# Performance work log

Hardware: AMD Instinct MI355X
Metric: run time of the kernel (lower is better)

The kernel has to match this reference:

```python
import jax, jax.numpy as jnp
import numpy as np

B, T, C, H, HS = 128, 256, 384, 6, 64

def setup_inputs() -> dict:
    key = jax.random.key(0)
    k1, k2, k3, k4, k5 = jax.random.split(key, 5)
    s = 0.02
    return {
        "x": jax.random.normal(k1, (B, T, C), dtype=jnp.float32),
        "Wq": jax.random.normal(k2, (H, C, HS), dtype=jnp.float32) * s,
        "Wk": jax.random.normal(k3, (H, C, HS), dtype=jnp.float32) * s,
        "Wv": jax.random.normal(k4, (H, C, HS), dtype=jnp.float32) * s,
        "Wp": jax.random.normal(k5, (C, C), dtype=jnp.float32) * s,
        "bp": jnp.zeros((C,), dtype=jnp.float32),
    }

def reference(x, Wq, Wk, Wv, Wp, bp):
    # per-head projections: [B,H,T,HS]
    q = jnp.einsum('btc,hcd->bhtd', x, Wq)
    k = jnp.einsum('btc,hcd->bhtd', x, Wk)
    v = jnp.einsum('btc,hcd->bhtd', x, Wv)
    scale = 1.0 / jnp.sqrt(jnp.asarray(HS, dtype=x.dtype))
    # scores: [B,H,T,T], causal mask then stable softmax
    scores = jnp.einsum('bhtd,bhsd->bhts', q, k) * scale
    causal = jnp.tril(jnp.ones((T, T), dtype=bool))
    scores = jnp.where(causal, scores, -jnp.inf)
    wei = jax.nn.softmax(scores, axis=-1)
    # dropout is identity in eval mode
    out = jnp.einsum('bhts,bhsd->bhtd', wei, v)  # [B,H,T,HS]
    out = out.transpose(0, 2, 1, 3).reshape(B, T, H * HS)  # concat heads
    return out @ Wp.T + bp  # output projection
```

## Files before the change

### kernel.cpp

```cpp
#include <hip/hip_runtime.h>
#include <hip/hip_bf16.h>
#include <math.h>

#define B_   128
#define T_   256
#define C_   384
#define H_   6
#define HS_  64
#define NTOK (B_*T_)
#define NQKV (3*C_)

typedef unsigned short u16;
typedef __attribute__((ext_vector_type(8))) short bf16x8;
typedef __attribute__((ext_vector_type(4))) float f32x4;

__device__ __forceinline__ u16 f2b(float f) {
    unsigned int u = __builtin_bit_cast(unsigned int, f);
    unsigned int r = (u + 0x7FFFu + ((u >> 16) & 1u)) >> 16;
    return (u16)r;
}

__device__ __forceinline__ float fexp2(float x) {
#if __has_builtin(__builtin_amdgcn_exp2f)
    return __builtin_amdgcn_exp2f(x);
#else
    return exp2f(x);
#endif
}

__device__ __forceinline__ void gl2lds16(const u16* g, u16* l) {
    __builtin_amdgcn_global_load_lds(
        (const __attribute__((address_space(1))) unsigned int*)g,
        (__attribute__((address_space(3))) unsigned int*)l, 16, 0, 0);
}

#define QSCALE 0.180336880f

#define J0_ (NTOK*C_/8)
#define J2_ (C_*C_/8)
#define J1_ (NQKV*C_)

__global__ __launch_bounds__(256) void prep(
    const float* __restrict__ x,  const float* __restrict__ Wq,
    const float* __restrict__ Wk, const float* __restrict__ Wv,
    const float* __restrict__ Wp,
    u16* __restrict__ xb, u16* __restrict__ wct, u16* __restrict__ wpb)
{
    int i = blockIdx.x * 256 + threadIdx.x;
    if (i < J0_) {
        const float4* s = (const float4*)x + (size_t)i * 2;
        float4 a = s[0], b = s[1];
        ushort4 o1, o2;
        o1.x = f2b(a.x); o1.y = f2b(a.y); o1.z = f2b(a.z); o1.w = f2b(a.w);
        o2.x = f2b(b.x); o2.y = f2b(b.y); o2.z = f2b(b.z); o2.w = f2b(b.w);
        ((ushort4*)xb)[(size_t)i * 2]     = o1;
        ((ushort4*)xb)[(size_t)i * 2 + 1] = o2;
    } else if (i < J0_ + J2_) {
        int j = i - J0_;
        const float4* s = (const float4*)Wp + (size_t)j * 2;
        float4 a = s[0], b = s[1];
        ushort4 o1, o2;
        o1.x = f2b(a.x); o1.y = f2b(a.y); o1.z = f2b(a.z); o1.w = f2b(a.w);
        o2.x = f2b(b.x); o2.y = f2b(b.y); o2.z = f2b(b.z); o2.w = f2b(b.w);
        ((ushort4*)wpb)[(size_t)j * 2]     = o1;
        ((ushort4*)wpb)[(size_t)j * 2 + 1] = o2;
    } else {
        int j = i - J0_ - J2_;
        if (j < J1_) {
            int n = j / C_, c = j % C_;
            int h = n / 192, rem = n % 192;
            int p = rem >> 6, d = rem & 63;
            const float* W = (p == 0 ? Wq : (p == 1 ? Wk : Wv));
            wct[j] = f2b(W[(h * C_ + c) * HS_ + d]);
        }
    }
}

__global__ __launch_bounds__(512, 2) void qkv_attn(
    const u16* __restrict__ xb, const u16* __restrict__ wct,
    u16* __restrict__ yb)
{
    __shared__ __align__(16) u16 SM[40960];
    u16* R0 = SM;
    u16* R1 = SM + 16384;
    u16* R2 = SM + 32768;

    const int gid = blockIdx.x;
    const int lin = (gid & 7) * 96 + (gid >> 3);
    const int b = lin / 6, h = lin % 6;

    const int tid = threadIdx.x;
    const int w = tid >> 6, lane = tid & 63;
    const int lm = lane & 15, qd = lane >> 4;
    const int wm = (w >> 1) * 64, wn = (w & 1) * 96;

    const int schunk = (lane & 7) ^ ((lane >> 3) & 7);
    const u16* gA = xb  + (size_t)(b * T_ + w * 32 + (lane >> 3)) * C_ + schunk * 8;
    const u16* gB = wct + (size_t)(h * 192 + w * 24 + (lane >> 3)) * C_ + schunk * 8;
    u16* lA = &R0[(w * 32) * 64];
    u16* lB = &R1[(w * 24) * 64];

    f32x4 acc[4][6];
    #pragma unroll
    for (int mi = 0; mi < 4; ++mi)
        #pragma unroll
        for (int ni = 0; ni < 6; ++ni)
            acc[mi][ni] = (f32x4){0.f, 0.f, 0.f, 0.f};

    for (int k0 = 0; k0 < C_; k0 += 64) {
        __syncthreads();
        #pragma unroll
        for (int j = 0; j < 4; ++j)
            gl2lds16(gA + j * 8 * C_, lA + j * 8 * 64);
        #pragma unroll
        for (int j = 0; j < 3; ++j)
            gl2lds16(gB + j * 8 * C_, lB + j * 8 * 64);
        gA += 64; gB += 64;
        __syncthreads();

        #pragma unroll
        for (int ks = 0; ks < 2; ++ks) {
            bf16x8 af[4], bfr[6];
            #pragma unroll
            for (int mi = 0; mi < 4; ++mi) {
                const int row = wm + mi * 16 + lm;
                const int sl = (ks * 4 + qd) ^ (lm & 7);
                af[mi] = *(const bf16x8*)&R0[row * 64 + sl * 8];
            }
            #pragma unroll
            for (int ni = 0; ni < 6; ++ni) {
                const int row = wn + ni * 16 + lm;
                const int sl = (ks * 4 + qd) ^ (lm & 7);
                bfr[ni] = *(const bf16x8*)&R1[row * 64 + sl * 8];
            }
            #pragma unroll
            for (int mi = 0; mi < 4; ++mi)
                #pragma unroll
                for (int ni = 0; ni < 6; ++ni)
                    acc[mi][ni] = __builtin_amdgcn_mfma_f32_16x16x32_bf16(
                        af[mi], bfr[ni], acc[mi][ni], 0, 0, 0);
        }
    }

    __syncthreads();
    #pragma unroll
    for (int mi = 0; mi < 4; ++mi) {
        const int t0 = wm + mi * 16 + qd * 4;
        #pragma unroll
        for (int ni = 0; ni < 6; ++ni) {
            const int n = wn + ni * 16 + lm;
            if (n < 64) {
                #pragma unroll
                for (int r = 0; r < 4; ++r) {
                    const int t = t0 + r;
                    R1[t * 64 + (((n >> 3) ^ (t & 7)) << 3) + (n & 7)]
                        = f2b(acc[mi][ni][r] * QSCALE);
                }
            } else if (n >= 128) {
                const int d = n - 128;
                const int ch = t0 >> 3;
                const int pos = (ch & 16) | ((ch ^ (d & 15)) & 15);
                ushort4 sv;
                sv.x = f2b(acc[mi][ni][0]); sv.y = f2b(acc[mi][ni][1]);
                sv.z = f2b(acc[mi][ni][2]); sv.w = f2b(acc[mi][ni][3]);
                *(ushort4*)&R0[d * 256 + pos * 8 + (t0 & 7)] = sv;
            }
        }
    }
    __syncthreads();

    const int trg0 = w * 16;
    const int trg1 = 128 + (7 - w) * 16;
    bf16x8 aq[2][2];
    #pragma unroll
    for (int rg = 0; rg < 2; ++rg) {
        const int t = (rg ? trg1 : trg0) + lm;
        #pragma unroll
        for (int ks = 0; ks < 2; ++ks)
            aq[rg][ks] = *(const bf16x8*)
                &R1[t * 64 + (((ks * 4 + qd) ^ (t & 7)) << 3)];
    }
    __syncthreads();

    #pragma unroll
    for (int mi = 0; mi < 4; ++mi) {
        const int t0 = wm + mi * 16 + qd * 4;
        #pragma unroll
        for (int ni = 0; ni < 6; ++ni) {
            const int n = wn + ni * 16 + lm;
            if (n >= 64 && n < 128) {
                const int d = n - 64;
                #pragma unroll
                for (int r = 0; r < 4; ++r) {
                    const int t = t0 + r;
                    R1[t * 64 + (((d >> 3) ^ (t & 7)) << 3) + (d & 7)]
                        = f2b(acc[mi][ni][r]);
                }
            }
        }
    }
    __syncthreads();

    f32x4 oacc[2][4];
    float ms[2][4], ls[2][4];
    #pragma unroll
    for (int rg = 0; rg < 2; ++rg) {
        #pragma unroll
        for (int ni = 0; ni < 4; ++ni) oacc[rg][ni] = (f32x4){0.f, 0.f, 0.f, 0.f};
        #pragma unroll
        for (int r = 0; r < 4; ++r) { ms[rg][r] = -INFINITY; ls[rg][r] = 0.f; }
    }

    u16* Pw = R2 + w * 1024;

    #pragma unroll
    for (int rg = 0; rg < 2; ++rg) {
        const int trg = rg ? trg1 : trg0;
        const int kmax = (trg + 15) >> 6;
        for (int kt = 0; kt <= kmax; ++kt) {
            const int j0 = kt * 64;
            const bool needmask = (j0 + 63 > trg);

            f32x4 st[4];
            #pragma unroll
            for (int ni = 0; ni < 4; ++ni) st[ni] = (f32x4){0.f, 0.f, 0.f, 0.f};
            #pragma unroll
            for (int ks = 0; ks < 2; ++ks) {
                #pragma unroll
                for (int ni = 0; ni < 4; ++ni) {
                    const int krow = j0 + ni * 16 + lm;
                    const int sl = (ks * 4 + qd) ^ (lm & 7);
                    bf16x8 bk = *(const bf16x8*)&R1[krow * 64 + sl * 8];
                    st[ni] = __builtin_amdgcn_mfma_f32_16x16x32_bf16(
                        aq[rg][ks], bk, st[ni], 0, 0, 0);
                }
            }

            float vals[4][4], rowmax[4];
            #pragma unroll
            for (int r = 0; r < 4; ++r) rowmax[r] = -INFINITY;
            #pragma unroll
            for (int ni = 0; ni < 4; ++ni) {
                const int s_g = j0 + ni * 16 + lm;
                #pragma unroll
                for (int r = 0; r < 4; ++r) {
                    float sc = st[ni][r];
                    if (needmask) {
                        const int t_g = trg + qd * 4 + r;
                        sc = (s_g > t_g) ? -1e30f : sc;
                    }
                    vals[ni][r] = sc;
                    rowmax[r] = fmaxf(rowmax[r], sc);
                }
            }
            #pragma unroll
            for (int msk = 1; msk <= 8; msk <<= 1)
                #pragma unroll
                for (int r = 0; r < 4; ++r)
                    rowmax[r] = fmaxf(rowmax[r], __shfl_xor(rowmax[r], msk, 64));

            float corr[4], rowsum[4];
            #pragma unroll
            for (int r = 0; r < 4; ++r) {
                const float mn = fmaxf(ms[rg][r], rowmax[r]);
                corr[r] = fexp2(ms[rg][r] - mn);
                ms[rg][r] = mn;
                rowsum[r] = 0.f;
            }
            #pragma unroll
            for (int ni = 0; ni < 4; ++ni) {
                #pragma unroll
                for (int r = 0; r < 4; ++r) {
                    const float pv = fexp2(vals[ni][r] - ms[rg][r]);
                    rowsum[r] += pv;
                    const int prow = qd * 4 + r;
                    const int pcol = ni * 16 + lm;
                    const int pch  = (pcol >> 3) ^ (prow & 7);
                    Pw[prow * 64 + pch * 8 + (pcol & 7)] = f2b(pv);
                }
            }
            #pragma unroll
            for (int msk = 1; msk <= 8; msk <<= 1)
                #pragma unroll
                for (int r = 0; r < 4; ++r)
                    rowsum[r] += __shfl_xor(rowsum[r], msk, 64);
            #pragma unroll
            for (int r = 0; r < 4; ++r) ls[rg][r] = ls[rg][r] * corr[r] + rowsum[r];
            #pragma unroll
            for (int ni = 0; ni < 4; ++ni)
                #pragma unroll
                for (int r = 0; r < 4; ++r)
                    oacc[rg][ni][r] *= corr[r];

            #pragma unroll
            for (int ks = 0; ks < 2; ++ks) {
                const int rch = (ks * 4 + qd) ^ (lm & 7);
                bf16x8 pa = *(const bf16x8*)&Pw[lm * 64 + rch * 8];
                #pragma unroll
                for (int ni = 0; ni < 4; ++ni) {
                    const int d = ni * 16 + lm;
                    const int cj = kt * 8 + ks * 4 + qd;
                    const int pos = (cj & 16) | ((cj ^ (d & 15)) & 15);
                    bf16x8 bv = *(const bf16x8*)&R0[d * 256 + pos * 8];
                    oacc[rg][ni] = __builtin_amdgcn_mfma_f32_16x16x32_bf16(
                        pa, bv, oacc[rg][ni], 0, 0, 0);
                }
            }
        }
    }

    __syncthreads();
    u16 (*yt)[72] = (u16(*)[72])SM;
    #pragma unroll
    for (int rg = 0; rg < 2; ++rg) {
        const int trow = (rg ? trg1 : trg0) + qd * 4;
        #pragma unroll
        for (int r = 0; r < 4; ++r) {
            const float inv = 1.f / ls[rg][r];
            #pragma unroll
            for (int ni = 0; ni < 4; ++ni)
                yt[trow + r][ni * 16 + lm] = f2b(oacc[rg][ni][r] * inv);
        }
    }
    __syncthreads();
    #pragma unroll
    for (int rr = 0; rr < 4; ++rr) {
        const int row = rr * 64 + (tid >> 3);
        const int col = (tid & 7) * 8;
        bf16x8 vv = *(const bf16x8*)&yt[row][col];
        *(bf16x8*)(yb + ((size_t)(b * T_ + row)) * C_ + h * 64 + col) = vv;
    }
}

__global__ __launch_bounds__(512, 4) void gemm_proj(
    const u16* __restrict__ yb, const u16* __restrict__ wpb,
    const float* __restrict__ bp, float* __restrict__ out)
{
    __shared__ __align__(16) u16 SMEM[256 * 64 + 128 * 64];
    u16* As = SMEM;
    u16* Bs = SMEM + 256 * 64;

    const int gid  = blockIdx.x;
    const int xcd  = gid & 7;
    const int j_   = gid >> 3;
    const int colb = j_ % 3;
    const int rowb = (j_ / 3) * 8 + xcd;
    const int m0g  = rowb * 256;
    const int n0g  = colb * 128;

    const int tid = threadIdx.x;
    const int w = tid >> 6, lane = tid & 63;
    const int lm = lane & 15, qd = lane >> 4;
    const int wm = (w >> 1) * 64, wn = (w & 1) * 64;

    const int schunk = (lane & 7) ^ ((lane >> 3) & 7);
    const u16* gA = yb  + (size_t)(m0g + w * 32 + (lane >> 3)) * C_ + schunk * 8;
    const u16* gB = wpb + (size_t)(n0g + w * 16 + (lane >> 3)) * C_ + schunk * 8;
    u16* lA = &As[(w * 32) * 64];
    u16* lB = &Bs[(w * 16) * 64];

    f32x4 acc[4][4];
    #pragma unroll
    for (int mi = 0; mi < 4; ++mi)
        #pragma unroll
        for (int ni = 0; ni < 4; ++ni)
            acc[mi][ni] = (f32x4){0.f, 0.f, 0.f, 0.f};

    for (int k0 = 0; k0 < C_; k0 += 64) {
        __syncthreads();
        #pragma unroll
        for (int j = 0; j < 4; ++j)
            gl2lds16(gA + j * 8 * C_, lA + j * 8 * 64);
        #pragma unroll
        for (int j = 0; j < 2; ++j)
            gl2lds16(gB + j * 8 * C_, lB + j * 8 * 64);
        gA += 64; gB += 64;
        __syncthreads();

        #pragma unroll
        for (int ks = 0; ks < 2; ++ks) {
            bf16x8 af[4], bfr[4];
            #pragma unroll
            for (int mi = 0; mi < 4; ++mi) {
                const int row = wm + mi * 16 + lm;
                const int sl = (ks * 4 + qd) ^ (lm & 7);
                af[mi] = *(const bf16x8*)&As[row * 64 + sl * 8];
            }
            #pragma unroll
            for (int ni = 0; ni < 4; ++ni) {
                const int row = wn + ni * 16 + lm;
                const int sl = (ks * 4 + qd) ^ (lm & 7);
                bfr[ni] = *(const bf16x8*)&Bs[row * 64 + sl * 8];
            }
            #pragma unroll
            for (int mi = 0; mi < 4; ++mi)
                #pragma unroll
                for (int ni = 0; ni < 4; ++ni)
                    acc[mi][ni] = __builtin_amdgcn_mfma_f32_16x16x32_bf16(
                        af[mi], bfr[ni], acc[mi][ni], 0, 0, 0);
        }
    }

    float bpv[4];
    #pragma unroll
    for (int ni = 0; ni < 4; ++ni) bpv[ni] = bp[n0g + wn + ni * 16 + lm];

    float (*tb)[132] = (float(*)[132])SMEM;
    const int rloc = tid >> 3;
    #pragma unroll
    for (int mi = 0; mi < 4; ++mi) {
        __syncthreads();
        #pragma unroll
        for (int ni = 0; ni < 4; ++ni)
            #pragma unroll
            for (int r = 0; r < 4; ++r)
                tb[(w >> 1) * 16 + qd * 4 + r][wn + ni * 16 + lm]
                    = acc[mi][ni][r] + bpv[ni];
        __syncthreads();
        const int m = m0g + (rloc >> 4) * 64 + mi * 16 + (rloc & 15);
        #pragma unroll
        for (int jj = 0; jj < 4; ++jj) {
            const int cc = (tid & 7) * 4 + jj * 32;
            float4 vv = *(const float4*)&tb[rloc][cc];
            *(float4*)(out + (size_t)m * C_ + n0g + cc) = vv;
        }
    }
}

extern "C" void kernel_launch(void* const* d_in, const int* in_sizes, int n_in,
                              void* d_out, int out_size, void* d_ws, size_t ws_size,
                              hipStream_t stream)
{
    const float* x  = (const float*)d_in[0];
    const float* Wq = (const float*)d_in[1];
    const float* Wk = (const float*)d_in[2];
    const float* Wv = (const float*)d_in[3];
    const float* Wp = (const float*)d_in[4];
    const float* bp = (const float*)d_in[5];
    float* out = (float*)d_out;

    u16* xb  = (u16*)d_ws;
    u16* wct = xb  + (size_t)NTOK * C_;
    u16* wpb = wct + (size_t)NQKV * C_;
    u16* yb  = wpb + (size_t)C_ * C_;

    const int prep_blocks = (J0_ + J2_ + J1_ + 255) / 256;
    hipLaunchKernelGGL(prep, dim3(prep_blocks), dim3(256), 0, stream,
                       x, Wq, Wk, Wv, Wp, xb, wct, wpb);

    hipLaunchKernelGGL(qkv_attn, dim3(B_ * H_), dim3(512), 0, stream,
                       xb, wct, yb);

    hipLaunchKernelGGL(gemm_proj, dim3((NTOK / 256) * (C_ / 128)), dim3(512), 0, stream,
                       yb, wpb, bp, out);
}
```

Measured before the change: 188.6 us.

## Double-buffer QKV GEMM loads, prefetch QK^T scores, use packed bf16 conversions

The QKV projection loop now double-buffers the x and weight tiles in LDS and uses explicit vmcnt waits, so global-to-LDS loads overlap the MFMA work instead of sitting behind two full barriers per step. Q, K and V are written to separate LDS regions in a single pass, which removes a sync-and-rewrite phase. The attention loop computes the next QK^T tile while the current softmax runs, and the fp32-to-bf16 rounding moves to the hardware packed convert, with rcp replacing division in the final normalisation. LDS use grows to 128 KB per block, which may cut occupancy from two blocks per CU to one.

```diff
diff --git a/kernel.cpp b/kernel.cpp
--- a/kernel.cpp
+++ b/kernel.cpp
@@ -18,6 +18,12 @@
     unsigned int u = __builtin_bit_cast(unsigned int, f);
     unsigned int r = (u + 0x7FFFu + ((u >> 16) & 1u)) >> 16;
     return (u16)r;
+}
+
+__device__ __forceinline__ unsigned pk2(float a, float b) {
+    unsigned r;
+    asm("v_cvt_pk_bf16_f32 %0, %1, %2" : "=v"(r) : "v"(a), "v"(b));
+    return r;
 }
 
 __device__ __forceinline__ float fexp2(float x) {
@@ -80,10 +86,15 @@
     const u16* __restrict__ xb, const u16* __restrict__ wct,
     u16* __restrict__ yb)
 {
-    __shared__ __align__(16) u16 SM[40960];
-    u16* R0 = SM;
-    u16* R1 = SM + 16384;
-    u16* R2 = SM + 32768;
+    __shared__ __align__(16) u16 SM[65536];
+    u16* A0 = SM;
+    u16* A1 = SM + 16384;
+    u16* B0 = SM + 32768;
+    u16* B1 = SM + 45056;
+    u16* Qs = SM;
+    u16* Vs = SM + 16384;
+    u16* Ks = SM + 32768;
+    u16* Pr = SM + 57344;
 
     const int gid = blockIdx.x;
     const int lin = (gid & 7) * 96 + (gid >> 3);
@@ -95,10 +106,10 @@
     const int wm = (w >> 1) * 64, wn = (w & 1) * 96;
 
     const int schunk = (lane & 7) ^ ((lane >> 3) & 7);
-    const u16* gA = xb  + (size_t)(b * T_ + w * 32 + (lane >> 3)) * C_ + schunk * 8;
-    const u16* gB = wct + (size_t)(h * 192 + w * 24 + (lane >> 3)) * C_ + schunk * 8;
-    u16* lA = &R0[(w * 32) * 64];
-    u16* lB = &R1[(w * 24) * 64];
+    const u16* gA0 = xb  + (size_t)(b * T_ + w * 32 + (lane >> 3)) * C_ + schunk * 8;
+    const u16* gB0 = wct + (size_t)(h * 192 + w * 24 + (lane >> 3)) * C_ + schunk * 8;
+    u16* lA[2] = { A0 + (w * 32) * 64, A1 + (w * 32) * 64 };
+    u16* lB[2] = { B0 + (w * 24) * 64, B1 + (w * 24) * 64 };
 
     f32x4 acc[4][6];
     #pragma unroll
@@ -107,16 +118,23 @@
         for (int ni = 0; ni < 6; ++ni)
             acc[mi][ni] = (f32x4){0.f, 0.f, 0.f, 0.f};
 
-    for (int k0 = 0; k0 < C_; k0 += 64) {
-        __syncthreads();
+    #pragma unroll
+    for (int s = 0; s < 2; ++s) {
         #pragma unroll
         for (int j = 0; j < 4; ++j)
-            gl2lds16(gA + j * 8 * C_, lA + j * 8 * 64);
+            gl2lds16(gA0 + s * 64 + j * 8 * C_, lA[s] + j * 8 * 64);
         #pragma unroll
         for (int j = 0; j < 3; ++j)
-            gl2lds16(gB + j * 8 * C_, lB + j * 8 * 64);
-        gA += 64; gB += 64;
-        __syncthreads();
+            gl2lds16(gB0 + s * 64 + j * 8 * C_, lB[s] + j * 8 * 64);
+    }
+
+    #pragma unroll
+    for (int k0i = 0; k0i < 6; ++k0i) {
+        if (k0i < 5) asm volatile("s_waitcnt vmcnt(7)" ::: "memory");
+        else         asm volatile("s_waitcnt vmcnt(0)" ::: "memory");
+        __builtin_amdgcn_s_barrier();
+        const u16* Ab = (k0i & 1) ? A1 : A0;
+        const u16* Bb = (k0i & 1) ? B1 : B0;
 
         #pragma unroll
         for (int ks = 0; ks < 2; ++ks) {
@@ -125,13 +143,13 @@
             for (int mi = 0; mi < 4; ++mi) {
                 const int row = wm + mi * 16 + lm;
                 const int sl = (ks * 4 + qd) ^ (lm & 7);
-                af[mi] = *(const bf16x8*)&R0[row * 64 + sl * 8];
+                af[mi] = *(const bf16x8*)&Ab[row * 64 + sl * 8];
             }
             #pragma unroll
             for (int ni = 0; ni < 6; ++ni) {
                 const int row = wn + ni * 16 + lm;
                 const int sl = (ks * 4 + qd) ^ (lm & 7);
-                bfr[ni] = *(const bf16x8*)&R1[row * 64 + sl * 8];
+                bfr[ni] = *(const bf16x8*)&Bb[row * 64 + sl * 8];
             }
             #pragma unroll
             for (int mi = 0; mi < 4; ++mi)
@@ -140,30 +158,56 @@
                     acc[mi][ni] = __builtin_amdgcn_mfma_f32_16x16x32_bf16(
                         af[mi], bfr[ni], acc[mi][ni], 0, 0, 0);
         }
+        asm volatile("" ::: "memory");
+        __builtin_amdgcn_s_barrier();
+        if (k0i < 4) {
+            #pragma unroll
+            for (int j = 0; j < 4; ++j)
+                gl2lds16(gA0 + (k0i + 2) * 64 + j * 8 * C_, lA[k0i & 1] + j * 8 * 64);
+            #pragma unroll
+            for (int j = 0; j < 3; ++j)
+                gl2lds16(gB0 + (k0i + 2) * 64 + j * 8 * C_, lB[k0i & 1] + j * 8 * 64);
+        }
     }
 
     __syncthreads();
+    const int wnu = __builtin_amdgcn_readfirstlane(wn);
     #pragma unroll
     for (int mi = 0; mi < 4; ++mi) {
         const int t0 = wm + mi * 16 + qd * 4;
         #pragma unroll
         for (int ni = 0; ni < 6; ++ni) {
+            const int cat = wnu + ni * 16;
             const int n = wn + ni * 16 + lm;
-            if (n < 64) {
+            if (cat < 64) {
+                unsigned p0 = pk2(acc[mi][ni][0] * QSCALE, acc[mi][ni][1] * QSCALE);
+                unsigned p1 = pk2(acc[mi][ni][2] * QSCALE, acc[mi][ni][3] * QSCALE);
                 #pragma unroll
                 for (int r = 0; r < 4; ++r) {
                     const int t = t0 + r;
-                    R1[t * 64 + (((n >> 3) ^ (t & 7)) << 3) + (n & 7)]
-                        = f2b(acc[mi][ni][r] * QSCALE);
+                    const unsigned pv = (r < 2) ? p0 : p1;
+                    Qs[t * 64 + (((n >> 3) ^ (t & 7)) << 3) + (n & 7)]
+                        = (r & 1) ? (u16)(pv >> 16) : (u16)pv;
                 }
-            } else if (n >= 128) {
+            } else if (cat < 128) {
+                const int d = n - 64;
+                unsigned p0 = pk2(acc[mi][ni][0], acc[mi][ni][1]);
+                unsigned p1 = pk2(acc[mi][ni][2], acc[mi][ni][3]);
+                #pragma unroll
+                for (int r = 0; r < 4; ++r) {
+                    const int t = t0 + r;
+                    const unsigned pv = (r < 2) ? p0 : p1;
+                    Ks[t * 64 + (((d >> 3) ^ (t & 7)) << 3) + (d & 7)]
+                        = (r & 1) ? (u16)(pv >> 16) : (u16)pv;
+                }
+            } else {
                 const int d = n - 128;
                 const int ch = t0 >> 3;
                 const int pos = (ch & 16) | ((ch ^ (d & 15)) & 15);
-                ushort4 sv;
-                sv.x = f2b(acc[mi][ni][0]); sv.y = f2b(acc[mi][ni][1]);
-                sv.z = f2b(acc[mi][ni][2]); sv.w = f2b(acc[mi][ni][3]);
-                *(ushort4*)&R0[d * 256 + pos * 8 + (t0 & 7)] = sv;
+                unsigned p0 = pk2(acc[mi][ni][0], acc[mi][ni][1]);
+                unsigned p1 = pk2(acc[mi][ni][2], acc[mi][ni][3]);
+                unsigned* dst = (unsigned*)&Vs[d * 256 + pos * 8 + (t0 & 7)];
+                dst[0] = p0; dst[1] = p1;
             }
         }
     }
@@ -178,28 +222,8 @@
         #pragma unroll
         for (int ks = 0; ks < 2; ++ks)
             aq[rg][ks] = *(const bf16x8*)
-                &R1[t * 64 + (((ks * 4 + qd) ^ (t & 7)) << 3)];
-    }
-    __syncthreads();
-
-    #pragma unroll
-    for (int mi = 0; mi < 4; ++mi) {
-        const int t0 = wm + mi * 16 + qd * 4;
-        #pragma unroll
-        for (int ni = 0; ni < 6; ++ni) {
-            const int n = wn + ni * 16 + lm;
-            if (n >= 64 && n < 128) {
-                const int d = n - 64;
-                #pragma unroll
-                for (int r = 0; r < 4; ++r) {
-                    const int t = t0 + r;
-                    R1[t * 64 + (((d >> 3) ^ (t & 7)) << 3) + (d & 7)]
-                        = f2b(acc[mi][ni][r]);
-                }
-            }
-        }
-    }
-    __syncthreads();
+                &Qs[t * 64 + (((ks * 4 + qd) ^ (t & 7)) << 3)];
+    }
 
     f32x4 oacc[2][4];
     float ms[2][4], ls[2][4];
@@ -211,30 +235,40 @@
         for (int r = 0; r < 4; ++r) { ms[rg][r] = -INFINITY; ls[rg][r] = 0.f; }
     }
 
-    u16* Pw = R2 + w * 1024;
+    u16* Pw = Pr + w * 1024;
+
+#define QKT16(ST, AQ, J0V)                                                    \
+    do {                                                                      \
+        _Pragma("unroll")                                                     \
+        for (int ni_ = 0; ni_ < 4; ++ni_) ST[ni_] = (f32x4){0.f,0.f,0.f,0.f}; \
+        _Pragma("unroll")                                                     \
+        for (int ks_ = 0; ks_ < 2; ++ks_) {                                   \
+            _Pragma("unroll")                                                 \
+            for (int ni_ = 0; ni_ < 4; ++ni_) {                               \
+                const int krow_ = (J0V) + ni_ * 16 + lm;                      \
+                const int sl_ = (ks_ * 4 + qd) ^ (lm & 7);                    \
+                bf16x8 bk_ = *(const bf16x8*)&Ks[krow_ * 64 + sl_ * 8];       \
+                ST[ni_] = __builtin_amdgcn_mfma_f32_16x16x32_bf16(            \
+                    AQ[ks_], bk_, ST[ni_], 0, 0, 0);                          \
+            }                                                                 \
+        }                                                                     \
+    } while (0)
 
     #pragma unroll
     for (int rg = 0; rg < 2; ++rg) {
         const int trg = rg ? trg1 : trg0;
-        const int kmax = (trg + 15) >> 6;
+        const int kmax = trg >> 6;
+
+        f32x4 stc[4];
+        QKT16(stc, aq[rg], 0);
+
         for (int kt = 0; kt <= kmax; ++kt) {
             const int j0 = kt * 64;
-            const bool needmask = (j0 + 63 > trg);
-
-            f32x4 st[4];
-            #pragma unroll
-            for (int ni = 0; ni < 4; ++ni) st[ni] = (f32x4){0.f, 0.f, 0.f, 0.f};
-            #pragma unroll
-            for (int ks = 0; ks < 2; ++ks) {
-                #pragma unroll
-                for (int ni = 0; ni < 4; ++ni) {
-                    const int krow = j0 + ni * 16 + lm;
-                    const int sl = (ks * 4 + qd) ^ (lm & 7);
-                    bf16x8 bk = *(const bf16x8*)&R1[krow * 64 + sl * 8];
-                    st[ni] = __builtin_amdgcn_mfma_f32_16x16x32_bf16(
-                        aq[rg][ks], bk, st[ni], 0, 0, 0);
-                }
-            }
+            const bool needmask = (kt == kmax);
+
+            f32x4 stn[4];
+            if (kt < kmax)
+                QKT16(stn, aq[rg], j0 + 64);
 
             float vals[4][4], rowmax[4];
             #pragma unroll
@@ -244,7 +278,7 @@
                 const int s_g = j0 + ni * 16 + lm;
                 #pragma unroll
                 for (int r = 0; r < 4; ++r) {
-                    float sc = st[ni][r];
+                    float sc = stc[ni][r];
                     if (needmask) {
                         const int t_g = trg + qd * 4 + r;
                         sc = (s_g > t_g) ? -1e30f : sc;
@@ -269,14 +303,21 @@
             }
             #pragma unroll
             for (int ni = 0; ni < 4; ++ni) {
+                float pv[4];
                 #pragma unroll
                 for (int r = 0; r < 4; ++r) {
-                    const float pv = fexp2(vals[ni][r] - ms[rg][r]);
-                    rowsum[r] += pv;
+                    pv[r] = fexp2(vals[ni][r] - ms[rg][r]);
+                    rowsum[r] += pv[r];
+                }
+                const int pcol = ni * 16 + lm;
+                unsigned p01 = pk2(pv[0], pv[1]);
+                unsigned p23 = pk2(pv[2], pv[3]);
+                #pragma unroll
+                for (int r = 0; r < 4; ++r) {
                     const int prow = qd * 4 + r;
-                    const int pcol = ni * 16 + lm;
-                    const int pch  = (pcol >> 3) ^ (prow & 7);
-                    Pw[prow * 64 + pch * 8 + (pcol & 7)] = f2b(pv);
+                    const unsigned pp = (r < 2) ? p01 : p23;
+                    Pw[prow * 64 + (((pcol >> 3) ^ (prow & 7)) << 3) + (pcol & 7)]
+                        = (r & 1) ? (u16)(pp >> 16) : (u16)pp;
                 }
             }
             #pragma unroll
@@ -301,11 +342,16 @@
                     const int d = ni * 16 + lm;
                     const int cj = kt * 8 + ks * 4 + qd;
                     const int pos = (cj & 16) | ((cj ^ (d & 15)) & 15);
-                    bf16x8 bv = *(const bf16x8*)&R0[d * 256 + pos * 8];
+                    bf16x8 bv = *(const bf16x8*)&Vs[d * 256 + pos * 8];
                     oacc[rg][ni] = __builtin_amdgcn_mfma_f32_16x16x32_bf16(
                         pa, bv, oacc[rg][ni], 0, 0, 0);
                 }
             }
+
+            if (kt < kmax) {
+                #pragma unroll
+                for (int ni = 0; ni < 4; ++ni) stc[ni] = stn[ni];
+            }
         }
     }
 
@@ -314,12 +360,18 @@
     #pragma unroll
     for (int rg = 0; rg < 2; ++rg) {
         const int trow = (rg ? trg1 : trg0) + qd * 4;
-        #pragma unroll
-        for (int r = 0; r < 4; ++r) {
-            const float inv = 1.f / ls[rg][r];
-            #pragma unroll
-            for (int ni = 0; ni < 4; ++ni)
-                yt[trow + r][ni * 16 + lm] = f2b(oacc[rg][ni][r] * inv);
+        float inv[4];
+        #pragma unroll
+        for (int r = 0; r < 4; ++r) inv[r] = __builtin_amdgcn_rcpf(ls[rg][r]);
+        #pragma unroll
+        for (int ni = 0; ni < 4; ++ni) {
+            unsigned p01 = pk2(oacc[rg][ni][0] * inv[0], oacc[rg][ni][1] * inv[1]);
+            unsigned p23 = pk2(oacc[rg][ni][2] * inv[2], oacc[rg][ni][3] * inv[3]);
+            #pragma unroll
+            for (int r = 0; r < 4; ++r) {
+                const unsigned pp = (r < 2) ? p01 : p23;
+                yt[trow + r][ni * 16 + lm] = (r & 1) ? (u16)(pp >> 16) : (u16)pp;
+            }
         }
     }
     __syncthreads();
```

New measurement: 181.0 us. -4.1%, faster.
